# Kernel optimization log

Hardware: AMD Instinct MI355X
Metric: run time of the kernel (lower is better)

Reference implementation:

```python
import jax, jax.numpy as jnp
import numpy as np

N_NODES = 100000
N_EDGES = 640000
D_IN = 128
D_OUT = 128


def setup_inputs() -> dict:
    key = jax.random.key(0)
    k_x, k_w, k_v, k_r, k_c = jax.random.split(key, 5)
    x = jax.random.normal(k_x, (N_NODES, D_IN), dtype=jnp.float32)
    # Xavier-uniform init for weights, zeros for bias (matches module init)
    limit = float(np.sqrt(6.0 / (D_IN + D_OUT)))
    weights = jax.random.uniform(k_w, (D_IN, D_OUT), dtype=jnp.float32,
                                 minval=-limit, maxval=limit)
    bias = jnp.zeros((D_OUT,), dtype=jnp.float32)
    # Sparse normalized adjacency in COO form: value[e] * y[col[e]] scattered to row[e]
    edge_val = jax.random.uniform(k_v, (N_EDGES,), dtype=jnp.float32)
    row = jax.random.randint(k_r, (N_EDGES,), 0, N_NODES, dtype=jnp.int32)
    col = jax.random.randint(k_c, (N_EDGES,), 0, N_NODES, dtype=jnp.int32)
    return {"x": x, "weights": weights, "bias": bias,
            "edge_val": edge_val, "row": row, "col": col}


def reference(x, weights, bias, edge_val, row, col):
    # y = x @ W  (dense GEMM)  [N, D_OUT]
    y = x @ weights
    # SpMM: out[i] = sum_{e: row[e]==i} edge_val[e] * y[col[e]]
    msg = edge_val[:, None] * y[col]            # [E, D_OUT] irregular gather
    agg = jax.ops.segment_sum(msg, row, num_segments=x.shape[0])
    return agg + bias
```

## Files before the change

kernel.cpp:

```cpp
#include <hip/hip_runtime.h>
#include <hip/hip_bf16.h>


#define N_NODES 100000
#define N_EDGES 640000
#define D 128
#define ELL_K 16
#define OVF_CAP 8192
#define NB 391
#define BCAP 2048
#define CHUNK 4096
#define NCHUNKS 157

typedef __attribute__((ext_vector_type(8))) short short8;
typedef __attribute__((ext_vector_type(4))) float f32x4;
typedef __attribute__((ext_vector_type(4))) ushort us4;

__device__ __forceinline__ ushort f2bf(float f) {
    uint u = __float_as_uint(f);
    u += 0x7fff + ((u >> 16) & 1);
    return (ushort)(u >> 16);
}
__device__ __forceinline__ float bflo(uint u) { return __uint_as_float(u << 16); }
__device__ __forceinline__ float bfhi(uint u) { return __uint_as_float(u & 0xffff0000u); }

__global__ __launch_bounds__(256, 2) void gemm_xw(const float* __restrict__ x,
                                                  const float* __restrict__ w,
                                                  ushort* __restrict__ y,
                                                  int* __restrict__ bucketCursor,
                                                  int* __restrict__ ovfCnt) {
    __shared__ ushort wt[128 * 128];
    const int tid = threadIdx.x;

    int gz = blockIdx.x * 256 + tid;
    if (gz < NB) bucketCursor[gz] = gz * BCAP;
    if (gz == 0) *ovfCnt = 0;

    #pragma unroll
    for (int it = 0; it < 16; ++it) {
        int idx4 = tid + it * 256;
        int k = idx4 >> 5;
        int n0 = (idx4 & 31) * 4;
        float4 v = *(const float4*)(w + (size_t)idx4 * 4);
        float vv[4] = {v.x, v.y, v.z, v.w};
        #pragma unroll
        for (int q = 0; q < 4; ++q) {
            int n = n0 + q;
            wt[n * 128 + (k ^ ((n & 7) << 3))] = f2bf(vv[q]);
        }
    }
    __syncthreads();

    const int lane = tid & 63;
    const int l15 = lane & 15;
    const int h = lane >> 4;

    short8 bfr[8][4];
    #pragma unroll
    for (int j = 0; j < 8; ++j) {
        int n = 16 * j + l15;
        #pragma unroll
        for (int ks = 0; ks < 4; ++ks) {
            int k0 = 32 * ks + 8 * h;
            bfr[j][ks] = *(const short8*)&wt[n * 128 + (k0 ^ ((n & 7) << 3))];
        }
    }

    const int waveGlobal = blockIdx.x * 4 + (tid >> 6);
    const int nWaves = gridDim.x * 4;
    const int nTiles = N_NODES / 16;

    for (int t = waveGlobal; t < nTiles; t += nWaves) {
        const float* xr = x + (size_t)(t * 16 + l15) * D;
        float4 xb[8];
        #pragma unroll
        for (int ks = 0; ks < 4; ++ks) {
            xb[2 * ks]     = *(const float4*)(xr + 32 * ks + 8 * h);
            xb[2 * ks + 1] = *(const float4*)(xr + 32 * ks + 8 * h + 4);
        }
        f32x4 acc[8];
        #pragma unroll
        for (int j = 0; j < 8; ++j) acc[j] = (f32x4){0.f, 0.f, 0.f, 0.f};
        #pragma unroll
        for (int ks = 0; ks < 4; ++ks) {
            const float* p0 = (const float*)&xb[2 * ks];
            const float* p1 = (const float*)&xb[2 * ks + 1];
            short8 a;
            a[0] = f2bf(p0[0]); a[1] = f2bf(p0[1]); a[2] = f2bf(p0[2]); a[3] = f2bf(p0[3]);
            a[4] = f2bf(p1[0]); a[5] = f2bf(p1[1]); a[6] = f2bf(p1[2]); a[7] = f2bf(p1[3]);
            #pragma unroll
            for (int j = 0; j < 8; ++j)
                acc[j] = __builtin_amdgcn_mfma_f32_16x16x32_bf16(bfr[j][ks], a, acc[j], 0, 0, 0);
        }
        ushort* yn = y + (size_t)(t * 16 + l15) * D;
        #pragma unroll
        for (int j = 0; j < 8; ++j) {
            us4 o;
            o.x = f2bf(acc[j][0]); o.y = f2bf(acc[j][1]);
            o.z = f2bf(acc[j][2]); o.w = f2bf(acc[j][3]);
            *(us4*)(yn + 16 * j + 4 * h) = o;
        }
    }
}

__global__ __launch_bounds__(256) void partition_edges(const float* __restrict__ ev,
                                                       const int* __restrict__ row,
                                                       const int* __restrict__ col,
                                                       int* __restrict__ bucketCursor,
                                                       uint2* __restrict__ es0,
                                                       int* __restrict__ ovfCnt,
                                                       int* __restrict__ ovfRow,
                                                       int* __restrict__ ovfCol,
                                                       float* __restrict__ ovfVal) {
    __shared__ int hist[NB];
    __shared__ int cur[NB];
    const int tid = threadIdx.x;
    const int base = blockIdx.x * CHUNK;

    for (int t = tid; t < NB; t += 256) hist[t] = 0;
    __syncthreads();

    #pragma unroll
    for (int it = 0; it < CHUNK / 256; ++it) {
        int i = base + it * 256 + tid;
        if (i < N_EDGES) atomicAdd(&hist[row[i] >> 8], 1);
    }
    __syncthreads();

    for (int t = tid; t < NB; t += 256) {
        int hcnt = hist[t];
        cur[t] = (hcnt > 0) ? atomicAdd(&bucketCursor[t], hcnt) : 0;
    }
    __syncthreads();

    #pragma unroll
    for (int it = 0; it < CHUNK / 256; ++it) {
        int i = base + it * 256 + tid;
        if (i < N_EDGES) {
            int r = row[i];
            int b = r >> 8;
            int p = atomicAdd(&cur[b], 1);
            if (p < (b + 1) * BCAP) {
                uint2 e;
                e.x = __float_as_uint(ev[i]);
                e.y = (uint)col[i] | ((uint)(r & 255) << 20);
                es0[p] = e;
            } else {
                int q = atomicAdd(ovfCnt, 1);
                if (q < OVF_CAP) {
                    ovfRow[q] = r;
                    ovfCol[q] = col[i];
                    ovfVal[q] = ev[i];
                }
            }
        }
    }
}

__global__ __launch_bounds__(256) void build_ell(const uint2* __restrict__ es0,
                                                 const int* __restrict__ bucketCursor,
                                                 float2* __restrict__ es,
                                                 int* __restrict__ counts,
                                                 int* __restrict__ ovfCnt,
                                                 int* __restrict__ ovfRow,
                                                 int* __restrict__ ovfCol,
                                                 float* __restrict__ ovfVal) {
    __shared__ float2 ell[256 * ELL_K];
    __shared__ int lcnt[256];
    const int tid = threadIdx.x;
    const int b = blockIdx.x;

    lcnt[tid] = 0;
    __syncthreads();

    int cnt = bucketCursor[b] - b * BCAP;
    if (cnt > BCAP) cnt = BCAP;
    const uint2* src = es0 + (size_t)b * BCAP;

    for (int i = tid; i < cnt; i += 256) {
        uint2 e = src[i];
        int r = e.y >> 20;
        int p = atomicAdd(&lcnt[r], 1);
        if (p < ELL_K) {
            float2 rec;
            rec.x = __uint_as_float(e.x);
            rec.y = __uint_as_float(e.y & 0xFFFFFu);
            ell[r * ELL_K + p] = rec;
        } else {
            int q = atomicAdd(ovfCnt, 1);
            if (q < OVF_CAP) {
                ovfRow[q] = b * 256 + r;
                ovfCol[q] = (int)(e.y & 0xFFFFFu);
                ovfVal[q] = __uint_as_float(e.x);
            }
        }
    }
    __syncthreads();

    const int nbase = b * 256;
    int nvalid = N_NODES - nbase;
    if (nvalid > 256) nvalid = 256;

    if (tid < nvalid) counts[nbase + tid] = lcnt[tid];

    float4* dst4 = (float4*)(es + (size_t)nbase * ELL_K);
    const float4* ell4 = (const float4*)ell;
    for (int t = tid; t < nvalid * (ELL_K / 2); t += 256)
        dst4[t] = ell4[t];
}

__global__ __launch_bounds__(256) void spmm_ell(const ushort* __restrict__ y,
                                                const float2* __restrict__ es,
                                                const int* __restrict__ counts,
                                                const float* __restrict__ bias,
                                                float* __restrict__ out) {
    const int tid = threadIdx.x;
    const int lane = tid & 63;
    const int wid = blockIdx.x * 4 + (tid >> 6);
    const float2 b2 = *(const float2*)(bias + lane * 2);

    #pragma unroll 1
    for (int rep = 0; rep < 2; ++rep) {
        const int n = __builtin_amdgcn_readfirstlane(wid * 2 + rep);
        int deg = counts[n];
        if (deg > ELL_K) deg = ELL_K;
        const float4* er = (const float4*)(es + (size_t)n * ELL_K);

        float ax = 0.f, ay = 0.f;
        #pragma unroll
        for (int g = 0; g < 4; ++g) {
            if (4 * g < deg) {
                float4 sA = er[2 * g];
                float4 sB = er[2 * g + 1];
                int c0 = __float_as_int(sA.y);
                int c1 = (4 * g + 1 < deg) ? __float_as_int(sA.w) : c0;
                int c2 = (4 * g + 2 < deg) ? __float_as_int(sB.y) : c0;
                int c3 = (4 * g + 3 < deg) ? __float_as_int(sB.w) : c0;
                uint u0 = *(const uint*)(y + ((size_t)c0 << 7) + lane * 2);
                uint u1 = *(const uint*)(y + ((size_t)c1 << 7) + lane * 2);
                uint u2 = *(const uint*)(y + ((size_t)c2 << 7) + lane * 2);
                uint u3 = *(const uint*)(y + ((size_t)c3 << 7) + lane * 2);
                float v0 = sA.x;
                float v1 = (4 * g + 1 < deg) ? sA.z : 0.f;
                float v2 = (4 * g + 2 < deg) ? sB.x : 0.f;
                float v3 = (4 * g + 3 < deg) ? sB.z : 0.f;
                ax += v0 * bflo(u0); ay += v0 * bfhi(u0);
                ax += v1 * bflo(u1); ay += v1 * bfhi(u1);
                ax += v2 * bflo(u2); ay += v2 * bfhi(u2);
                ax += v3 * bflo(u3); ay += v3 * bfhi(u3);
            }
        }
        float2 o = {ax + b2.x, ay + b2.y};
        *(float2*)(out + ((size_t)n << 7) + lane * 2) = o;
    }
}

__global__ void ovf_fix(const ushort* __restrict__ y, const int* __restrict__ ovfRow,
                        const int* __restrict__ ovfCol, const float* __restrict__ ovfVal,
                        const int* __restrict__ ovfCnt, float* __restrict__ out) {
    int nOvf = *ovfCnt;
    if (nOvf > OVF_CAP) nOvf = OVF_CAP;
    int total = nOvf * 32;
    for (int idx = blockIdx.x * 256 + threadIdx.x; idx < total; idx += gridDim.x * 256) {
        int e = idx >> 5;
        int c = idx & 31;
        int r = ovfRow[e];
        int col = ovfCol[e];
        float v = ovfVal[e];
        uint2 u = *(const uint2*)(y + ((size_t)col << 7) + c * 4);
        atomicAdd(&out[(size_t)r * D + c * 4 + 0], v * bflo(u.x));
        atomicAdd(&out[(size_t)r * D + c * 4 + 1], v * bfhi(u.x));
        atomicAdd(&out[(size_t)r * D + c * 4 + 2], v * bflo(u.y));
        atomicAdd(&out[(size_t)r * D + c * 4 + 3], v * bfhi(u.y));
    }
}

extern "C" void kernel_launch(void* const* d_in, const int* in_sizes, int n_in,
                              void* d_out, int out_size, void* d_ws, size_t ws_size,
                              hipStream_t stream) {
    const float* x = (const float*)d_in[0];
    const float* w = (const float*)d_in[1];
    const float* bias = (const float*)d_in[2];
    const float* ev = (const float*)d_in[3];
    const int* row = (const int*)d_in[4];
    const int* col = (const int*)d_in[5];
    float* out = (float*)d_out;

    size_t off = 0;
    auto carve = [&](size_t bytes) -> void* {
        void* p = (char*)d_ws + off;
        off += (bytes + 255) & ~(size_t)255;
        return p;
    };
    ushort* y = (ushort*)carve((size_t)N_NODES * D * sizeof(ushort));
    int* counts = (int*)carve((size_t)N_NODES * sizeof(int));
    float2* es = (float2*)carve((size_t)N_NODES * ELL_K * sizeof(float2));
    uint2* es0 = (uint2*)carve((size_t)NB * BCAP * sizeof(uint2));
    int* bucketCursor = (int*)carve(NB * sizeof(int));
    int* ovfCnt = (int*)carve(sizeof(int));
    int* ovfRow = (int*)carve(OVF_CAP * sizeof(int));
    int* ovfCol = (int*)carve(OVF_CAP * sizeof(int));
    float* ovfVal = (float*)carve(OVF_CAP * sizeof(float));

    gemm_xw<<<512, 256, 0, stream>>>(x, w, y, bucketCursor, ovfCnt);
    partition_edges<<<NCHUNKS, 256, 0, stream>>>(ev, row, col, bucketCursor, es0,
                                                 ovfCnt, ovfRow, ovfCol, ovfVal);
    build_ell<<<NB, 256, 0, stream>>>(es0, bucketCursor, es, counts,
                                      ovfCnt, ovfRow, ovfCol, ovfVal);
    spmm_ell<<<N_NODES / 8, 256, 0, stream>>>(y, es, counts, bias, out);
    ovf_fix<<<16, 256, 0, stream>>>(y, ovfRow, ovfCol, ovfVal, ovfCnt, out);
}
```

Baseline: 85.75 us.

## Pad ELL with zeros, drop degree counts, widen SpMM gathers, raise GEMM occupancy

```diff
diff --git a/kernel.cpp b/kernel.cpp
--- a/kernel.cpp
+++ b/kernel.cpp
@@ -9,8 +9,10 @@
 #define OVF_CAP 8192
 #define NB 391
 #define BCAP 2048
-#define CHUNK 4096
-#define NCHUNKS 157
+#define CHUNK 2048
+#define NCHUNKS 313
+#define N_TILES 6250
+#define ELL_P 17
 
 typedef __attribute__((ext_vector_type(8))) short short8;
 typedef __attribute__((ext_vector_type(4))) float f32x4;
@@ -24,17 +26,15 @@
 __device__ __forceinline__ float bflo(uint u) { return __uint_as_float(u << 16); }
 __device__ __forceinline__ float bfhi(uint u) { return __uint_as_float(u & 0xffff0000u); }
 
-__global__ __launch_bounds__(256, 2) void gemm_xw(const float* __restrict__ x,
+__global__ __launch_bounds__(256, 4) void gemm_xw(const float* __restrict__ x,
                                                   const float* __restrict__ w,
                                                   ushort* __restrict__ y,
-                                                  int* __restrict__ bucketCursor,
-                                                  int* __restrict__ ovfCnt) {
+                                                  int* __restrict__ bucketCnt) {
     __shared__ ushort wt[128 * 128];
     const int tid = threadIdx.x;
 
     int gz = blockIdx.x * 256 + tid;
-    if (gz < NB) bucketCursor[gz] = gz * BCAP;
-    if (gz == 0) *ovfCnt = 0;
+    if (gz <= NB) bucketCnt[gz] = 0;
 
     #pragma unroll
     for (int it = 0; it < 16; ++it) {
@@ -55,22 +55,11 @@
     const int l15 = lane & 15;
     const int h = lane >> 4;
 
-    short8 bfr[8][4];
-    #pragma unroll
-    for (int j = 0; j < 8; ++j) {
-        int n = 16 * j + l15;
-        #pragma unroll
-        for (int ks = 0; ks < 4; ++ks) {
-            int k0 = 32 * ks + 8 * h;
-            bfr[j][ks] = *(const short8*)&wt[n * 128 + (k0 ^ ((n & 7) << 3))];
-        }
-    }
-
     const int waveGlobal = blockIdx.x * 4 + (tid >> 6);
     const int nWaves = gridDim.x * 4;
-    const int nTiles = N_NODES / 16;
-
-    for (int t = waveGlobal; t < nTiles; t += nWaves) {
+
+    for (int t = waveGlobal; t < N_TILES; t += nWaves) {
+        asm volatile("" ::: "memory");
         const float* xr = x + (size_t)(t * 16 + l15) * D;
         float4 xb[8];
         #pragma unroll
@@ -78,19 +67,28 @@
             xb[2 * ks]     = *(const float4*)(xr + 32 * ks + 8 * h);
             xb[2 * ks + 1] = *(const float4*)(xr + 32 * ks + 8 * h + 4);
         }
-        f32x4 acc[8];
-        #pragma unroll
-        for (int j = 0; j < 8; ++j) acc[j] = (f32x4){0.f, 0.f, 0.f, 0.f};
+        short8 a[4];
         #pragma unroll
         for (int ks = 0; ks < 4; ++ks) {
             const float* p0 = (const float*)&xb[2 * ks];
             const float* p1 = (const float*)&xb[2 * ks + 1];
-            short8 a;
-            a[0] = f2bf(p0[0]); a[1] = f2bf(p0[1]); a[2] = f2bf(p0[2]); a[3] = f2bf(p0[3]);
-            a[4] = f2bf(p1[0]); a[5] = f2bf(p1[1]); a[6] = f2bf(p1[2]); a[7] = f2bf(p1[3]);
+            a[ks][0] = f2bf(p0[0]); a[ks][1] = f2bf(p0[1]);
+            a[ks][2] = f2bf(p0[2]); a[ks][3] = f2bf(p0[3]);
+            a[ks][4] = f2bf(p1[0]); a[ks][5] = f2bf(p1[1]);
+            a[ks][6] = f2bf(p1[2]); a[ks][7] = f2bf(p1[3]);
+        }
+        f32x4 acc[8];
+        #pragma unroll
+        for (int j = 0; j < 8; ++j) acc[j] = (f32x4){0.f, 0.f, 0.f, 0.f};
+        #pragma unroll
+        for (int ks = 0; ks < 4; ++ks) {
+            const int k0 = 32 * ks + 8 * h;
             #pragma unroll
-            for (int j = 0; j < 8; ++j)
-                acc[j] = __builtin_amdgcn_mfma_f32_16x16x32_bf16(bfr[j][ks], a, acc[j], 0, 0, 0);
+            for (int j = 0; j < 8; ++j) {
+                int n = 16 * j + l15;
+                short8 b = *(const short8*)&wt[n * 128 + (k0 ^ ((n & 7) << 3))];
+                acc[j] = __builtin_amdgcn_mfma_f32_16x16x32_bf16(b, a[ks], acc[j], 0, 0, 0);
+            }
         }
         ushort* yn = y + (size_t)(t * 16 + l15) * D;
         #pragma unroll
@@ -106,7 +104,7 @@
 __global__ __launch_bounds__(256) void partition_edges(const float* __restrict__ ev,
                                                        const int* __restrict__ row,
                                                        const int* __restrict__ col,
-                                                       int* __restrict__ bucketCursor,
+                                                       int* __restrict__ bucketCnt,
                                                        uint2* __restrict__ es0,
                                                        int* __restrict__ ovfCnt,
                                                        int* __restrict__ ovfRow,
@@ -128,8 +126,9 @@
     __syncthreads();
 
     for (int t = tid; t < NB; t += 256) {
-        int hcnt = hist[t];
-        cur[t] = (hcnt > 0) ? atomicAdd(&bucketCursor[t], hcnt) : 0;
+        int h = hist[t];
+        int start = (h > 0) ? atomicAdd(&bucketCnt[t], h) : 0;
+        cur[t] = t * BCAP + start;
     }
     __syncthreads();
 
@@ -158,22 +157,24 @@
 }
 
 __global__ __launch_bounds__(256) void build_ell(const uint2* __restrict__ es0,
-                                                 const int* __restrict__ bucketCursor,
+                                                 const int* __restrict__ bucketCnt,
                                                  float2* __restrict__ es,
-                                                 int* __restrict__ counts,
                                                  int* __restrict__ ovfCnt,
                                                  int* __restrict__ ovfRow,
                                                  int* __restrict__ ovfCol,
                                                  float* __restrict__ ovfVal) {
-    __shared__ float2 ell[256 * ELL_K];
+    __shared__ float2 ell[256 * ELL_P];
     __shared__ int lcnt[256];
     const int tid = threadIdx.x;
     const int b = blockIdx.x;
 
     lcnt[tid] = 0;
-    __syncthreads();
-
-    int cnt = bucketCursor[b] - b * BCAP;
+    #pragma unroll
+    for (int it = 0; it < ELL_P; ++it)
+        ell[it * 256 + tid] = (float2){0.f, 0.f};
+    __syncthreads();
+
+    int cnt = bucketCnt[b];
     if (cnt > BCAP) cnt = BCAP;
     const uint2* src = es0 + (size_t)b * BCAP;
 
@@ -185,7 +186,7 @@
             float2 rec;
             rec.x = __uint_as_float(e.x);
             rec.y = __uint_as_float(e.y & 0xFFFFFu);
-            ell[r * ELL_K + p] = rec;
+            ell[r * ELL_P + p] = rec;
         } else {
             int q = atomicAdd(ovfCnt, 1);
             if (q < OVF_CAP) {
@@ -201,58 +202,52 @@
     int nvalid = N_NODES - nbase;
     if (nvalid > 256) nvalid = 256;
 
-    if (tid < nvalid) counts[nbase + tid] = lcnt[tid];
-
-    float4* dst4 = (float4*)(es + (size_t)nbase * ELL_K);
-    const float4* ell4 = (const float4*)ell;
-    for (int t = tid; t < nvalid * (ELL_K / 2); t += 256)
-        dst4[t] = ell4[t];
+    float2* dst2 = es + (size_t)nbase * ELL_K;
+    for (int t = tid; t < nvalid * ELL_K; t += 256) {
+        int r = t >> 4, s = t & 15;
+        dst2[t] = ell[r * ELL_P + s];
+    }
 }
 
 __global__ __launch_bounds__(256) void spmm_ell(const ushort* __restrict__ y,
                                                 const float2* __restrict__ es,
-                                                const int* __restrict__ counts,
                                                 const float* __restrict__ bias,
                                                 float* __restrict__ out) {
     const int tid = threadIdx.x;
-    const int lane = tid & 63;
-    const int wid = blockIdx.x * 4 + (tid >> 6);
-    const float2 b2 = *(const float2*)(bias + lane * 2);
-
-    #pragma unroll 1
-    for (int rep = 0; rep < 2; ++rep) {
-        const int n = __builtin_amdgcn_readfirstlane(wid * 2 + rep);
-        int deg = counts[n];
-        if (deg > ELL_K) deg = ELL_K;
-        const float4* er = (const float4*)(es + (size_t)n * ELL_K);
-
-        float ax = 0.f, ay = 0.f;
-        #pragma unroll
-        for (int g = 0; g < 4; ++g) {
-            if (4 * g < deg) {
-                float4 sA = er[2 * g];
-                float4 sB = er[2 * g + 1];
-                int c0 = __float_as_int(sA.y);
-                int c1 = (4 * g + 1 < deg) ? __float_as_int(sA.w) : c0;
-                int c2 = (4 * g + 2 < deg) ? __float_as_int(sB.y) : c0;
-                int c3 = (4 * g + 3 < deg) ? __float_as_int(sB.w) : c0;
-                uint u0 = *(const uint*)(y + ((size_t)c0 << 7) + lane * 2);
-                uint u1 = *(const uint*)(y + ((size_t)c1 << 7) + lane * 2);
-                uint u2 = *(const uint*)(y + ((size_t)c2 << 7) + lane * 2);
-                uint u3 = *(const uint*)(y + ((size_t)c3 << 7) + lane * 2);
-                float v0 = sA.x;
-                float v1 = (4 * g + 1 < deg) ? sA.z : 0.f;
-                float v2 = (4 * g + 2 < deg) ? sB.x : 0.f;
-                float v3 = (4 * g + 3 < deg) ? sB.z : 0.f;
-                ax += v0 * bflo(u0); ay += v0 * bfhi(u0);
-                ax += v1 * bflo(u1); ay += v1 * bfhi(u1);
-                ax += v2 * bflo(u2); ay += v2 * bfhi(u2);
-                ax += v3 * bflo(u3); ay += v3 * bfhi(u3);
-            }
-        }
-        float2 o = {ax + b2.x, ay + b2.y};
-        *(float2*)(out + ((size_t)n << 7) + lane * 2) = o;
-    }
+    const int c16 = tid & 15;
+    const int n = blockIdx.x * 16 + (tid >> 4);
+
+    const float4* er = (const float4*)(es + (size_t)n * ELL_K);
+    float4 e0 = er[0], e1 = er[1], e2 = er[2], e3 = er[3];
+    float4 e4 = er[4], e5 = er[5], e6 = er[6], e7 = er[7];
+
+    const ushort* yb = y + c16 * 8;
+    #define YLD(c) (*(const uint4*)(yb + ((size_t)__float_as_int(c) << 7)))
+    uint4 u0 = YLD(e0.y), u1 = YLD(e0.w), u2 = YLD(e1.y), u3 = YLD(e1.w);
+    uint4 u4 = YLD(e2.y), u5 = YLD(e2.w), u6 = YLD(e3.y), u7 = YLD(e3.w);
+    uint4 u8 = YLD(e4.y), u9 = YLD(e4.w), uA = YLD(e5.y), uB = YLD(e5.w);
+    uint4 uC = YLD(e6.y), uD = YLD(e6.w), uE = YLD(e7.y), uF = YLD(e7.w);
+    #undef YLD
+
+    float a[8] = {0.f, 0.f, 0.f, 0.f, 0.f, 0.f, 0.f, 0.f};
+    #define FMA8(v, u) do { \
+        a[0] += (v) * bflo((u).x); a[1] += (v) * bfhi((u).x); \
+        a[2] += (v) * bflo((u).y); a[3] += (v) * bfhi((u).y); \
+        a[4] += (v) * bflo((u).z); a[5] += (v) * bfhi((u).z); \
+        a[6] += (v) * bflo((u).w); a[7] += (v) * bfhi((u).w); } while (0)
+    FMA8(e0.x, u0); FMA8(e0.z, u1); FMA8(e1.x, u2); FMA8(e1.z, u3);
+    FMA8(e2.x, u4); FMA8(e2.z, u5); FMA8(e3.x, u6); FMA8(e3.z, u7);
+    FMA8(e4.x, u8); FMA8(e4.z, u9); FMA8(e5.x, uA); FMA8(e5.z, uB);
+    FMA8(e6.x, uC); FMA8(e6.z, uD); FMA8(e7.x, uE); FMA8(e7.z, uF);
+    #undef FMA8
+
+    const float4 b0 = *(const float4*)(bias + c16 * 8);
+    const float4 b1 = *(const float4*)(bias + c16 * 8 + 4);
+    float4 o0 = {a[0] + b0.x, a[1] + b0.y, a[2] + b0.z, a[3] + b0.w};
+    float4 o1 = {a[4] + b1.x, a[5] + b1.y, a[6] + b1.z, a[7] + b1.w};
+    float* orow = out + ((size_t)n << 7) + c16 * 8;
+    *(float4*)orow = o0;
+    *(float4*)(orow + 4) = o1;
 }
 
 __global__ void ovf_fix(const ushort* __restrict__ y, const int* __restrict__ ovfRow,
@@ -293,20 +288,19 @@
         return p;
     };
     ushort* y = (ushort*)carve((size_t)N_NODES * D * sizeof(ushort));
-    int* counts = (int*)carve((size_t)N_NODES * sizeof(int));
     float2* es = (float2*)carve((size_t)N_NODES * ELL_K * sizeof(float2));
     uint2* es0 = (uint2*)carve((size_t)NB * BCAP * sizeof(uint2));
-    int* bucketCursor = (int*)carve(NB * sizeof(int));
-    int* ovfCnt = (int*)carve(sizeof(int));
+    int* bucketCnt = (int*)carve((NB + 1) * sizeof(int));
+    int* ovfCnt = bucketCnt + NB;
     int* ovfRow = (int*)carve(OVF_CAP * sizeof(int));
     int* ovfCol = (int*)carve(OVF_CAP * sizeof(int));
     float* ovfVal = (float*)carve(OVF_CAP * sizeof(float));
 
-    gemm_xw<<<512, 256, 0, stream>>>(x, w, y, bucketCursor, ovfCnt);
-    partition_edges<<<NCHUNKS, 256, 0, stream>>>(ev, row, col, bucketCursor, es0,
+    gemm_xw<<<782, 256, 0, stream>>>(x, w, y, bucketCnt);
+    partition_edges<<<NCHUNKS, 256, 0, stream>>>(ev, row, col, bucketCnt, es0,
                                                  ovfCnt, ovfRow, ovfCol, ovfVal);
-    build_ell<<<NB, 256, 0, stream>>>(es0, bucketCursor, es, counts,
+    build_ell<<<NB, 256, 0, stream>>>(es0, bucketCnt, es,
                                       ovfCnt, ovfRow, ovfCol, ovfVal);
-    spmm_ell<<<N_NODES / 8, 256, 0, stream>>>(y, es, counts, bias, out);
+    spmm_ell<<<N_NODES / 16, 256, 0, stream>>>(y, es, bias, out);
     ovf_fix<<<16, 256, 0, stream>>>(y, ovfRow, ovfCol, ovfVal, ovfCnt, out);
 }
```

New measurement: 88.21 us. 2.9% more time.
